# Performance work log

Hardware: AMD Instinct MI355X
Metric: run time of the kernel (lower is better)

The kernel has to match this reference:

```python
import jax, jax.numpy as jnp
import numpy as np

A, B, SDIM, ADIM, H, NH, DH = 15, 32768, 128, 32, 128, 4, 32
NEG = -1e9

def _lrelu(x):
    return jax.nn.leaky_relu(x, 0.01)

def setup_inputs() -> dict:
    key = jax.random.key(0)
    ks = jax.random.split(key, 14)
    w = lambda k, shp, s=0.05: jax.random.normal(k, shp, dtype=jnp.float32) * s
    return {
        'states': jax.random.normal(ks[0], (A, B, SDIM), dtype=jnp.float32),
        'actions': jax.random.normal(ks[1], (A, B, ADIM), dtype=jnp.float32),
        'Wenc': w(ks[2], (A, SDIM + ADIM, H)),
        'benc': w(ks[3], (A, H)),
        'Wsenc': w(ks[4], (A, SDIM, H)),
        'bsenc': w(ks[5], (A, H)),
        'Wk': w(ks[6], (NH, H, DH)),
        'Wsel': w(ks[7], (NH, H, DH)),
        'Wv': w(ks[8], (NH, H, DH)),
        'bv': w(ks[9], (NH, DH)),
        'Wc1': w(ks[10], (A, 2 * H, H)),
        'bc1': w(ks[11], (A, H)),
        'Wc2': w(ks[12], (A, H, ADIM)),
        'bc2': w(ks[13], (A, ADIM)),
    }

def reference(states, actions, Wenc, benc, Wsenc, bsenc, Wk, Wsel, Wv, bv, Wc1, bc1, Wc2, bc2):
    # per-agent (obs, act) encoders: [A,B,idim] x [A,idim,H] -> [A,B,H]
    sa = jnp.concatenate([states, actions], axis=-1)
    sa_enc = _lrelu(jnp.einsum('abi,aih->abh', sa, Wenc) + benc[:, None, :])
    s_enc = _lrelu(jnp.einsum('abs,ash->abh', states, Wsenc) + bsenc[:, None, :])
    # per-head key/value/selector projections (shared across agents)
    keys = jnp.einsum('jbe,ned->jbnd', sa_enc, Wk)                      # [A,B,NH,DH]
    vals = _lrelu(jnp.einsum('jbe,ned->jbnd', sa_enc, Wv) + bv[None, None])
    sel = jnp.einsum('ibe,ned->ibnd', s_enc, Wsel)                      # [A,B,NH,DH]
    # exclude-self attention over other agents
    logits = jnp.einsum('ibnd,jbnd->ibnj', sel, keys) / np.sqrt(DH).astype(np.float32)
    self_mask = jnp.eye(A, dtype=bool)[:, None, None, :]                # [A,1,1,A]
    probs = jax.nn.softmax(jnp.where(self_mask, NEG, logits), axis=-1)  # [A,B,NH,A]
    attn = jnp.einsum('ibnj,jbnd->ibnd', probs, vals)                   # [A,B,NH,DH]
    # per-agent critic head: cat(s_enc, all-head attention values) -> Q over actions
    critic_in = jnp.concatenate([s_enc, attn.reshape(A, B, NH * DH)], axis=-1)  # [A,B,2H]
    h = _lrelu(jnp.einsum('abi,aih->abh', critic_in, Wc1) + bc1[:, None, :])
    all_q = jnp.einsum('abh,aho->abo', h, Wc2) + bc2[:, None, :]        # [A,B,ADIM]
    return all_q
```

## Files before the change

kernel.cpp:

```cpp
#include <hip/hip_runtime.h>

typedef unsigned short u16;
typedef __attribute__((ext_vector_type(8))) short short8;
typedef __attribute__((ext_vector_type(4))) float f32x4;

#define NB 32768

__device__ __forceinline__ u16 f2bf(float x){
  unsigned int u = __float_as_uint(x);
  u += 0x7fffu + ((u >> 16) & 1u);
  return (u16)(u >> 16);
}
__device__ __forceinline__ float bf2f(short h){
  return __uint_as_float(((unsigned int)(u16)h) << 16);
}
__device__ __forceinline__ short8 pack8(float4 a, float4 b){
  short8 p;
  p[0]=(short)f2bf(a.x); p[1]=(short)f2bf(a.y); p[2]=(short)f2bf(a.z); p[3]=(short)f2bf(a.w);
  p[4]=(short)f2bf(b.x); p[5]=(short)f2bf(b.y); p[6]=(short)f2bf(b.z); p[7]=(short)f2bf(b.w);
  return p;
}

__global__ __launch_bounds__(256) void k0_conv(
    const float* __restrict__ Wenc, const float* __restrict__ Wsenc,
    const float* __restrict__ Wk, const float* __restrict__ Wsel, const float* __restrict__ Wv,
    const float* __restrict__ Wc1, const float* __restrict__ Wc2,
    u16* __restrict__ WencB, u16* __restrict__ WsencB,
    u16* __restrict__ WkB, u16* __restrict__ WvB, u16* __restrict__ WselB,
    u16* __restrict__ Wc1B, u16* __restrict__ Wc2B)
{
  int idx = blockIdx.x * 256 + threadIdx.x;
  if (idx < 307200){
    int a = idx / 20480, r = idx % 20480, n = r / 160, k = r % 160;
    WencB[idx] = f2bf(Wenc[a*20480 + k*128 + n]);
  } else if (idx < 552960){
    int i = idx - 307200; int a = i / 16384, r = i % 16384, n = r / 128, k = r % 128;
    WsencB[i] = f2bf(Wsenc[a*16384 + k*128 + n]);
  } else if (idx < 569344){
    int i = idx - 552960; int c = i / 128, k = i % 128;
    WkB[i] = f2bf(Wk[(c>>5)*4096 + k*32 + (c&31)]);
  } else if (idx < 585728){
    int i = idx - 569344; int c = i / 128, k = i % 128;
    WvB[i] = f2bf(Wv[(c>>5)*4096 + k*32 + (c&31)]);
  } else if (idx < 602112){
    int i = idx - 585728; int c = i / 128, k = i % 128;
    WselB[i] = f2bf(Wsel[(c>>5)*4096 + k*32 + (c&31)]);
  } else if (idx < 1093632){
    int i = idx - 602112; int a = i / 32768, r = i % 32768, n = r / 256, k = r % 256;
    Wc1B[i] = f2bf(Wc1[a*32768 + k*128 + n]);
  } else if (idx < 1155072){
    int i = idx - 1093632; int a = i / 4096, r = i % 4096, n = r / 128, k = r % 128;
    Wc2B[i] = f2bf(Wc2[a*4096 + k*32 + n]);
  }
}

__device__ __forceinline__ short8 ldA(const char* lds, int off, int row, int slot){
  return *(const short8*)(lds + off + row*256 + ((slot ^ (row & 7)) << 4));
}
__device__ __forceinline__ void stSwz(char* lds, int off, int row, int col, u16 v){
  *(u16*)(lds + off + row*256 + ((((col>>3) ^ (row&7))) << 4) + ((col&7) << 1)) = v;
}
#define MFMA(a8,b8,c) __builtin_amdgcn_mfma_f32_16x16x32_bf16(a8, b8, c, 0, 0, 0)

__device__ __forceinline__ void k1_gemm128(
    char* B, const short8* A0, const short8* A1, const u16* __restrict__ W,
    const float* __restrict__ bias, bool act, int l15, int l4)
{
  #pragma unroll
  for (int c = 0; c < 8; ++c){
    int col = c*16 + l15;
    const u16* Wn = W + (size_t)col*128;
    f32x4 a0 = (f32x4)0.f, a1 = (f32x4)0.f;
    #pragma unroll
    for (int ks = 0; ks < 4; ++ks){
      short8 b8 = *(const short8*)(Wn + ks*32 + l4*8);
      a0 = MFMA(A0[ks], b8, a0);
      a1 = MFMA(A1[ks], b8, a1);
    }
    float bb = bias ? bias[col] : 0.0f;
    #pragma unroll
    for (int q = 0; q < 4; ++q){
      float v0 = a0[q] + bb, v1 = a1[q] + bb;
      if (act){ v0 = v0 > 0.f ? v0 : 0.01f*v0; v1 = v1 > 0.f ? v1 : 0.01f*v1; }
      stSwz(B, 0, l4*4 + q,      col, f2bf(v0));
      stSwz(B, 0, 16 + l4*4 + q, col, f2bf(v1));
    }
  }
}
__device__ __forceinline__ void k1_copyout(const char* B, u16* __restrict__ dst,
                                           int a, int m0, int lane)
{
  #pragma unroll
  for (int it = 0; it < 8; ++it){
    int e = lane + it*64, row = e >> 4, cb = e & 15;
    *(short8*)(dst + ((size_t)a*NB + m0 + row)*128 + cb*8) =
        *(const short8*)(B + row*256 + ((cb ^ (row&7)) << 4));
  }
}

__global__ __launch_bounds__(256, 2) void k1_enc(
    const float* __restrict__ states, const float* __restrict__ actions,
    const float* __restrict__ benc, const float* __restrict__ bsenc, const float* __restrict__ bvp,
    const u16* __restrict__ WencB, const u16* __restrict__ WsencB,
    const u16* __restrict__ WkB, const u16* __restrict__ WvB, const u16* __restrict__ WselB,
    u16* __restrict__ se_g, u16* __restrict__ keys_g, u16* __restrict__ vals_g, u16* __restrict__ sel_g)
{
  extern __shared__ __align__(16) char lds[];
  const int a = blockIdx.y;
  const int w = threadIdx.x >> 6, lane = threadIdx.x & 63;
  const int l15 = lane & 15, l4 = lane >> 4;
  const int m0 = blockIdx.x*128 + w*32;
  char* B = lds + w*8192;

  short8 s0[4], s1[4], aa0, aa1;
  #pragma unroll
  for (int ks = 0; ks < 4; ++ks){
    const float* p0 = states + ((size_t)a*NB + m0 + l15)*128 + ks*32 + l4*8;
    s0[ks] = pack8(*(const float4*)p0, *(const float4*)(p0 + 4));
    const float* p1 = p0 + 16*128;
    s1[ks] = pack8(*(const float4*)p1, *(const float4*)(p1 + 4));
  }
  {
    const float* q0 = actions + ((size_t)a*NB + m0 + l15)*32 + l4*8;
    aa0 = pack8(*(const float4*)q0, *(const float4*)(q0 + 4));
    const float* q1 = q0 + 16*32;
    aa1 = pack8(*(const float4*)q1, *(const float4*)(q1 + 4));
  }

  k1_gemm128(B, s0, s1, WsencB + (size_t)a*16384, bsenc + a*128, true, l15, l4);
  k1_copyout(B, se_g, a, m0, lane);
  short8 seA0[4], seA1[4];
  #pragma unroll
  for (int ks = 0; ks < 4; ++ks){
    seA0[ks] = ldA(B, 0, l15,      ks*4 + l4);
    seA1[ks] = ldA(B, 0, 16 + l15, ks*4 + l4);
  }

  {
    const u16* We = WencB + (size_t)a*20480;
    const float* bi = benc + a*128;
    #pragma unroll
    for (int c = 0; c < 8; ++c){
      int col = c*16 + l15;
      const u16* Wn = We + (size_t)col*160;
      f32x4 a0 = (f32x4)0.f, a1 = (f32x4)0.f;
      #pragma unroll
      for (int ks = 0; ks < 4; ++ks){
        short8 b8 = *(const short8*)(Wn + ks*32 + l4*8);
        a0 = MFMA(s0[ks], b8, a0);
        a1 = MFMA(s1[ks], b8, a1);
      }
      short8 bt = *(const short8*)(Wn + 128 + l4*8);
      a0 = MFMA(aa0, bt, a0);
      a1 = MFMA(aa1, bt, a1);
      float bb = bi[col];
      #pragma unroll
      for (int q = 0; q < 4; ++q){
        float v0 = a0[q] + bb, v1 = a1[q] + bb;
        v0 = v0 > 0.f ? v0 : 0.01f*v0; v1 = v1 > 0.f ? v1 : 0.01f*v1;
        stSwz(B, 0, l4*4 + q,      col, f2bf(v0));
        stSwz(B, 0, 16 + l4*4 + q, col, f2bf(v1));
      }
    }
  }
  short8 saA0[4], saA1[4];
  #pragma unroll
  for (int ks = 0; ks < 4; ++ks){
    saA0[ks] = ldA(B, 0, l15,      ks*4 + l4);
    saA1[ks] = ldA(B, 0, 16 + l15, ks*4 + l4);
  }

  k1_gemm128(B, saA0, saA1, WkB, (const float*)nullptr, false, l15, l4);
  k1_copyout(B, keys_g, a, m0, lane);
  k1_gemm128(B, saA0, saA1, WvB, bvp, true, l15, l4);
  k1_copyout(B, vals_g, a, m0, lane);
  k1_gemm128(B, seA0, seA1, WselB, (const float*)nullptr, false, l15, l4);
  k1_copyout(B, sel_g, a, m0, lane);
}

#define KO 0
#define VO 61440
#define K2A_LDS 122880

__global__ __launch_bounds__(1024) void k2a_attn(
    const u16* __restrict__ keys_g, const u16* __restrict__ vals_g,
    const u16* __restrict__ sel_g, u16* __restrict__ attn_g)
{
  extern __shared__ __align__(16) char lds[];
  const int b0 = blockIdx.x * 16;
  const int t = threadIdx.x;
  const int lane = t & 63, w = t >> 6;
  const int b = lane >> 2, h = lane & 3;
  const bool act = w < 15;

  float sf[32];
  size_t base = 0;
  if (act){
    base = ((size_t)w*NB + b0 + b)*128 + h*32;
    #pragma unroll
    for (int x = 0; x < 4; ++x){
      short8 s8 = *(const short8*)(sel_g + base + x*8);
      #pragma unroll
      for (int y = 0; y < 8; ++y) sf[x*8+y] = bf2f(s8[y]);
    }
  }
  for (int e = t; e < 3840; e += 1024){
    int row = e >> 4, cb = e & 15;
    size_t src = ((size_t)(row >> 4)*NB + b0 + (row & 15))*128 + cb*8;
    int dst = row*256 + ((cb ^ (row&7)) << 4);
    *(short8*)(lds + KO + dst) = *(const short8*)(keys_g + src);
    *(short8*)(lds + VO + dst) = *(const short8*)(vals_g + src);
  }
  __syncthreads();

  if (act){
    float lg[15];
    #pragma unroll
    for (int j = 0; j < 15; ++j){
      int row = j*16 + b;
      float d = 0.f;
      #pragma unroll
      for (int x = 0; x < 4; ++x){
        short8 k8 = *(const short8*)(lds + KO + row*256 + (((h*4 + x) ^ (row&7)) << 4));
        #pragma unroll
        for (int y = 0; y < 8; ++y) d += bf2f(k8[y]) * sf[x*8+y];
      }
      lg[j] = d * 0.17677669529663687f;
    }
    float mx = -1e30f;
    #pragma unroll
    for (int j = 0; j < 15; ++j) if (j != w) mx = fmaxf(mx, lg[j]);
    float sum = 0.f;
    #pragma unroll
    for (int j = 0; j < 15; ++j){
      float p = (j == w) ? 0.f : __expf(lg[j] - mx);
      lg[j] = p; sum += p;
    }
    float inv = 1.f / sum;
    float oa[32];
    #pragma unroll
    for (int x = 0; x < 32; ++x) oa[x] = 0.f;
    #pragma unroll
    for (int j = 0; j < 15; ++j){
      if (j == w) continue;
      float p = lg[j];
      int row = j*16 + b;
      #pragma unroll
      for (int x = 0; x < 4; ++x){
        short8 v8 = *(const short8*)(lds + VO + row*256 + (((h*4 + x) ^ (row&7)) << 4));
        #pragma unroll
        for (int y = 0; y < 8; ++y) oa[x*8+y] += p * bf2f(v8[y]);
      }
    }
    #pragma unroll
    for (int x = 0; x < 4; ++x){
      short8 o;
      #pragma unroll
      for (int y = 0; y < 8; ++y) o[y] = (short)f2bf(oa[x*8+y] * inv);
      *(short8*)(attn_g + base + x*8) = o;
    }
  }
}

__global__ __launch_bounds__(256, 2) void k2b_critic(
    const u16* __restrict__ se_g, const u16* __restrict__ attn_g,
    const u16* __restrict__ Wc1B, const u16* __restrict__ Wc2B,
    const float* __restrict__ bc1, const float* __restrict__ bc2,
    float* __restrict__ outp)
{
  extern __shared__ __align__(16) char lds[];
  const int a = blockIdx.y;
  const int w = threadIdx.x >> 6, lane = threadIdx.x & 63;
  const int l15 = lane & 15, l4 = lane >> 4;
  const int m0 = blockIdx.x*128 + w*32;
  char* B = lds + w*8192;

  short8 se0[4], se1[4], at0[4], at1[4];
  #pragma unroll
  for (int ks = 0; ks < 4; ++ks){
    size_t o0 = ((size_t)a*NB + m0 + l15)*128 + ks*32 + l4*8;
    size_t o1 = o0 + 16*128;
    se0[ks] = *(const short8*)(se_g + o0);
    se1[ks] = *(const short8*)(se_g + o1);
    at0[ks] = *(const short8*)(attn_g + o0);
    at1[ks] = *(const short8*)(attn_g + o1);
  }
  {
    const u16* Wc = Wc1B + (size_t)a*32768;
    const float* bi = bc1 + a*128;
    #pragma unroll
    for (int c = 0; c < 8; ++c){
      int col = c*16 + l15;
      const u16* Wn = Wc + (size_t)col*256;
      f32x4 a0 = (f32x4)0.f, a1 = (f32x4)0.f;
      #pragma unroll
      for (int ks = 0; ks < 4; ++ks){
        short8 b8 = *(const short8*)(Wn + ks*32 + l4*8);
        a0 = MFMA(se0[ks], b8, a0);
        a1 = MFMA(se1[ks], b8, a1);
      }
      #pragma unroll
      for (int ks = 0; ks < 4; ++ks){
        short8 b8 = *(const short8*)(Wn + 128 + ks*32 + l4*8);
        a0 = MFMA(at0[ks], b8, a0);
        a1 = MFMA(at1[ks], b8, a1);
      }
      float bb = bi[col];
      #pragma unroll
      for (int q = 0; q < 4; ++q){
        float v0 = a0[q] + bb, v1 = a1[q] + bb;
        v0 = v0 > 0.f ? v0 : 0.01f*v0; v1 = v1 > 0.f ? v1 : 0.01f*v1;
        stSwz(B, 0, l4*4 + q,      col, f2bf(v0));
        stSwz(B, 0, 16 + l4*4 + q, col, f2bf(v1));
      }
    }
  }
  short8 h0[4], h1[4];
  #pragma unroll
  for (int ks = 0; ks < 4; ++ks){
    h0[ks] = ldA(B, 0, l15,      ks*4 + l4);
    h1[ks] = ldA(B, 0, 16 + l15, ks*4 + l4);
  }
  #pragma unroll
  for (int fn = 0; fn < 2; ++fn){
    int col = fn*16 + l15;
    const u16* Wn = Wc2B + (size_t)a*4096 + (size_t)col*128;
    f32x4 a0 = (f32x4)0.f, a1 = (f32x4)0.f;
    #pragma unroll
    for (int ks = 0; ks < 4; ++ks){
      short8 b8 = *(const short8*)(Wn + ks*32 + l4*8);
      a0 = MFMA(h0[ks], b8, a0);
      a1 = MFMA(h1[ks], b8, a1);
    }
    float bb = bc2[a*32 + col];
    #pragma unroll
    for (int q = 0; q < 4; ++q){
      outp[((size_t)a*NB + m0 + l4*4 + q)*32 + col]      = a0[q] + bb;
      outp[((size_t)a*NB + m0 + 16 + l4*4 + q)*32 + col] = a1[q] + bb;
    }
  }
}

extern "C" void kernel_launch(void* const* d_in, const int* in_sizes, int n_in,
                              void* d_out, int out_size, void* d_ws, size_t ws_size,
                              hipStream_t stream)
{
  const float* states  = (const float*)d_in[0];
  const float* actions = (const float*)d_in[1];
  const float* Wenc    = (const float*)d_in[2];
  const float* benc    = (const float*)d_in[3];
  const float* Wsenc   = (const float*)d_in[4];
  const float* bsenc   = (const float*)d_in[5];
  const float* Wk      = (const float*)d_in[6];
  const float* Wsel    = (const float*)d_in[7];
  const float* Wv      = (const float*)d_in[8];
  const float* bv      = (const float*)d_in[9];
  const float* Wc1     = (const float*)d_in[10];
  const float* bc1     = (const float*)d_in[11];
  const float* Wc2     = (const float*)d_in[12];
  const float* bc2     = (const float*)d_in[13];

  char* ws = (char*)d_ws;
  u16* WencB  = (u16*)(ws + 0);
  u16* WsencB = (u16*)(ws + 614400);
  u16* WkB    = (u16*)(ws + 1105920);
  u16* WvB    = (u16*)(ws + 1138688);
  u16* WselB  = (u16*)(ws + 1171456);
  u16* Wc1B   = (u16*)(ws + 1204224);
  u16* Wc2B   = (u16*)(ws + 2187264);
  u16* se_g   = (u16*)(ws + 2310144);
  u16* keys_g = (u16*)(ws + 128139264);
  u16* vals_g = (u16*)(ws + 253968384);
  u16* sel_g  = (u16*)(ws + 379797504);
  if (ws_size < 505626624ULL) return;

  hipFuncSetAttribute((const void*)k1_enc,     hipFuncAttributeMaxDynamicSharedMemorySize, 32768);
  hipFuncSetAttribute((const void*)k2a_attn,   hipFuncAttributeMaxDynamicSharedMemorySize, K2A_LDS);
  hipFuncSetAttribute((const void*)k2b_critic, hipFuncAttributeMaxDynamicSharedMemorySize, 32768);

  k0_conv<<<4512, 256, 0, stream>>>(Wenc, Wsenc, Wk, Wsel, Wv, Wc1, Wc2,
                                    WencB, WsencB, WkB, WvB, WselB, Wc1B, Wc2B);
  k1_enc<<<dim3(256, 15), 256, 32768, stream>>>(states, actions, benc, bsenc, bv,
                                                WencB, WsencB, WkB, WvB, WselB,
                                                se_g, keys_g, vals_g, sel_g);
  k2a_attn<<<2048, 1024, K2A_LDS, stream>>>(keys_g, vals_g, sel_g, keys_g);
  k2b_critic<<<dim3(256, 15), 256, 32768, stream>>>(se_g, keys_g, Wc1B, Wc2B,
                                                    bc1, bc2, (float*)d_out);
}
```

Baseline: 657.9 us.

## Stage encoder and projection weights in LDS shared across waves in k1_enc

In k1_enc each block now loads each weight matrix cooperatively into a swizzled LDS buffer, with a separate tail region for the action columns of Wenc, and all four waves read B operands from LDS instead of each wave fetching them from global/L2. The GEMMs are reordered so the selector projection runs right after the state encoder, which frees the register arrays that held s_enc. The aim is to cut redundant weight traffic and register pressure. In exchange the kernel adds several block-wide barriers and raises LDS to 72KB per block, which may limit how many blocks fit per CU.

```diff
diff --git a/kernel.cpp b/kernel.cpp
--- a/kernel.cpp
+++ b/kernel.cpp
@@ -14,6 +14,7 @@
 __device__ __forceinline__ float bf2f(short h){
   return __uint_as_float(((unsigned int)(u16)h) << 16);
 }
+__device__ __forceinline__ float lrelu(float v){ return v > 0.f ? v : 0.01f*v; }
 __device__ __forceinline__ short8 pack8(float4 a, float4 b){
   short8 p;
   p[0]=(short)f2bf(a.x); p[1]=(short)f2bf(a.y); p[2]=(short)f2bf(a.z); p[3]=(short)f2bf(a.w);
@@ -62,18 +63,35 @@
 }
 #define MFMA(a8,b8,c) __builtin_amdgcn_mfma_f32_16x16x32_bf16(a8, b8, c, 0, 0, 0)
 
-__device__ __forceinline__ void k1_gemm128(
-    char* B, const short8* A0, const short8* A1, const u16* __restrict__ W,
+#define WBUF 0
+#define WTAIL 32768
+#define BOUNCE 40960
+#define K1_LDS 73728
+
+__device__ __forceinline__ void stageW(char* lds, const u16* __restrict__ W, int ldk, int t){
+  #pragma unroll
+  for (int i = 0; i < 8; ++i){
+    int e = t + i*256;
+    int col = e >> 4, slot = e & 15;
+    *(short8*)(lds + WBUF + col*256 + ((slot ^ (col&7)) << 4)) =
+        *(const short8*)(W + (size_t)col*ldk + slot*8);
+  }
+}
+__device__ __forceinline__ short8 ldB(const char* lds, int col, int slot){
+  return *(const short8*)(lds + WBUF + col*256 + ((slot ^ (col&7)) << 4));
+}
+
+__device__ __forceinline__ void gemm2L(
+    char* B, const char* lds, const short8* A0, const short8* A1,
     const float* __restrict__ bias, bool act, int l15, int l4)
 {
   #pragma unroll
   for (int c = 0; c < 8; ++c){
     int col = c*16 + l15;
-    const u16* Wn = W + (size_t)col*128;
     f32x4 a0 = (f32x4)0.f, a1 = (f32x4)0.f;
     #pragma unroll
     for (int ks = 0; ks < 4; ++ks){
-      short8 b8 = *(const short8*)(Wn + ks*32 + l4*8);
+      short8 b8 = ldB(lds, col, ks*4 + l4);
       a0 = MFMA(A0[ks], b8, a0);
       a1 = MFMA(A1[ks], b8, a1);
     }
@@ -81,7 +99,7 @@
     #pragma unroll
     for (int q = 0; q < 4; ++q){
       float v0 = a0[q] + bb, v1 = a1[q] + bb;
-      if (act){ v0 = v0 > 0.f ? v0 : 0.01f*v0; v1 = v1 > 0.f ? v1 : 0.01f*v1; }
+      if (act){ v0 = lrelu(v0); v1 = lrelu(v1); }
       stSwz(B, 0, l4*4 + q,      col, f2bf(v0));
       stSwz(B, 0, 16 + l4*4 + q, col, f2bf(v1));
     }
@@ -107,12 +125,13 @@
 {
   extern __shared__ __align__(16) char lds[];
   const int a = blockIdx.y;
-  const int w = threadIdx.x >> 6, lane = threadIdx.x & 63;
+  const int t = threadIdx.x;
+  const int w = t >> 6, lane = t & 63;
   const int l15 = lane & 15, l4 = lane >> 4;
   const int m0 = blockIdx.x*128 + w*32;
-  char* B = lds + w*8192;
-
-  short8 s0[4], s1[4], aa0, aa1;
+  char* B = lds + BOUNCE + w*8192;
+
+  short8 s0[4], s1[4];
   #pragma unroll
   for (int ks = 0; ks < 4; ++ks){
     const float* p0 = states + ((size_t)a*NB + m0 + l15)*128 + ks*32 + l4*8;
@@ -120,62 +139,81 @@
     const float* p1 = p0 + 16*128;
     s1[ks] = pack8(*(const float4*)p1, *(const float4*)(p1 + 4));
   }
+
+  short8 T0[4], T1[4];
+
+  stageW(lds, WsencB + (size_t)a*16384, 128, t);
+  __syncthreads();
+  gemm2L(B, lds, s0, s1, bsenc + a*128, true, l15, l4);
+  k1_copyout(B, se_g, a, m0, lane);
+  #pragma unroll
+  for (int ks = 0; ks < 4; ++ks){
+    T0[ks] = ldA(B, 0, l15,      ks*4 + l4);
+    T1[ks] = ldA(B, 0, 16 + l15, ks*4 + l4);
+  }
+  __syncthreads();
+
+  stageW(lds, WselB, 128, t);
+  __syncthreads();
+  gemm2L(B, lds, T0, T1, (const float*)nullptr, false, l15, l4);
+  k1_copyout(B, sel_g, a, m0, lane);
+  __syncthreads();
+
+  stageW(lds, WencB + (size_t)a*20480, 160, t);
+  #pragma unroll
+  for (int i = 0; i < 2; ++i){
+    int e = t + i*256;
+    int col = e >> 2, sl = e & 3;
+    *(short8*)(lds + WTAIL + col*64 + ((sl ^ (col&3)) << 4)) =
+        *(const short8*)(WencB + (size_t)a*20480 + (size_t)col*160 + 128 + sl*8);
+  }
+  __syncthreads();
   {
+    short8 aa0, aa1;
     const float* q0 = actions + ((size_t)a*NB + m0 + l15)*32 + l4*8;
     aa0 = pack8(*(const float4*)q0, *(const float4*)(q0 + 4));
     const float* q1 = q0 + 16*32;
     aa1 = pack8(*(const float4*)q1, *(const float4*)(q1 + 4));
-  }
-
-  k1_gemm128(B, s0, s1, WsencB + (size_t)a*16384, bsenc + a*128, true, l15, l4);
-  k1_copyout(B, se_g, a, m0, lane);
-  short8 seA0[4], seA1[4];
-  #pragma unroll
-  for (int ks = 0; ks < 4; ++ks){
-    seA0[ks] = ldA(B, 0, l15,      ks*4 + l4);
-    seA1[ks] = ldA(B, 0, 16 + l15, ks*4 + l4);
-  }
-
-  {
-    const u16* We = WencB + (size_t)a*20480;
     const float* bi = benc + a*128;
     #pragma unroll
     for (int c = 0; c < 8; ++c){
       int col = c*16 + l15;
-      const u16* Wn = We + (size_t)col*160;
       f32x4 a0 = (f32x4)0.f, a1 = (f32x4)0.f;
       #pragma unroll
       for (int ks = 0; ks < 4; ++ks){
-        short8 b8 = *(const short8*)(Wn + ks*32 + l4*8);
+        short8 b8 = ldB(lds, col, ks*4 + l4);
         a0 = MFMA(s0[ks], b8, a0);
         a1 = MFMA(s1[ks], b8, a1);
       }
-      short8 bt = *(const short8*)(Wn + 128 + l4*8);
+      short8 bt = *(const short8*)(lds + WTAIL + col*64 + ((l4 ^ (col&3)) << 4));
       a0 = MFMA(aa0, bt, a0);
       a1 = MFMA(aa1, bt, a1);
       float bb = bi[col];
       #pragma unroll
       for (int q = 0; q < 4; ++q){
         float v0 = a0[q] + bb, v1 = a1[q] + bb;
-        v0 = v0 > 0.f ? v0 : 0.01f*v0; v1 = v1 > 0.f ? v1 : 0.01f*v1;
-        stSwz(B, 0, l4*4 + q,      col, f2bf(v0));
-        stSwz(B, 0, 16 + l4*4 + q, col, f2bf(v1));
-      }
-    }
-  }
-  short8 saA0[4], saA1[4];
+        stSwz(B, 0, l4*4 + q,      col, f2bf(lrelu(v0)));
+        stSwz(B, 0, 16 + l4*4 + q, col, f2bf(lrelu(v1)));
+      }
+    }
+  }
   #pragma unroll
   for (int ks = 0; ks < 4; ++ks){
-    saA0[ks] = ldA(B, 0, l15,      ks*4 + l4);
-    saA1[ks] = ldA(B, 0, 16 + l15, ks*4 + l4);
-  }
-
-  k1_gemm128(B, saA0, saA1, WkB, (const float*)nullptr, false, l15, l4);
+    T0[ks] = ldA(B, 0, l15,      ks*4 + l4);
+    T1[ks] = ldA(B, 0, 16 + l15, ks*4 + l4);
+  }
+  __syncthreads();
+
+  stageW(lds, WkB, 128, t);
+  __syncthreads();
+  gemm2L(B, lds, T0, T1, (const float*)nullptr, false, l15, l4);
   k1_copyout(B, keys_g, a, m0, lane);
-  k1_gemm128(B, saA0, saA1, WvB, bvp, true, l15, l4);
+  __syncthreads();
+
+  stageW(lds, WvB, 128, t);
+  __syncthreads();
+  gemm2L(B, lds, T0, T1, bvp, true, l15, l4);
   k1_copyout(B, vals_g, a, m0, lane);
-  k1_gemm128(B, seA0, seA1, WselB, (const float*)nullptr, false, l15, l4);
-  k1_copyout(B, sel_g, a, m0, lane);
 }
 
 #define KO 0
@@ -309,7 +347,7 @@
       #pragma unroll
       for (int q = 0; q < 4; ++q){
         float v0 = a0[q] + bb, v1 = a1[q] + bb;
-        v0 = v0 > 0.f ? v0 : 0.01f*v0; v1 = v1 > 0.f ? v1 : 0.01f*v1;
+        v0 = lrelu(v0); v1 = lrelu(v1);
         stSwz(B, 0, l4*4 + q,      col, f2bf(v0));
         stSwz(B, 0, 16 + l4*4 + q, col, f2bf(v1));
       }
@@ -374,15 +412,15 @@
   u16* sel_g  = (u16*)(ws + 379797504);
   if (ws_size < 505626624ULL) return;
 
-  hipFuncSetAttribute((const void*)k1_enc,     hipFuncAttributeMaxDynamicSharedMemorySize, 32768);
+  hipFuncSetAttribute((const void*)k1_enc,     hipFuncAttributeMaxDynamicSharedMemorySize, K1_LDS);
   hipFuncSetAttribute((const void*)k2a_attn,   hipFuncAttributeMaxDynamicSharedMemorySize, K2A_LDS);
   hipFuncSetAttribute((const void*)k2b_critic, hipFuncAttributeMaxDynamicSharedMemorySize, 32768);
 
   k0_conv<<<4512, 256, 0, stream>>>(Wenc, Wsenc, Wk, Wsel, Wv, Wc1, Wc2,
                                     WencB, WsencB, WkB, WvB, WselB, Wc1B, Wc2B);
-  k1_enc<<<dim3(256, 15), 256, 32768, stream>>>(states, actions, benc, bsenc, bv,
-                                                WencB, WsencB, WkB, WvB, WselB,
-                                                se_g, keys_g, vals_g, sel_g);
+  k1_enc<<<dim3(256, 15), 256, K1_LDS, stream>>>(states, actions, benc, bsenc, bv,
+                                                 WencB, WsencB, WkB, WvB, WselB,
+                                                 se_g, keys_g, vals_g, sel_g);
   k2a_attn<<<2048, 1024, K2A_LDS, stream>>>(keys_g, vals_g, sel_g, keys_g);
   k2b_critic<<<dim3(256, 15), 256, 32768, stream>>>(se_g, keys_g, Wc1B, Wc2B,
                                                     bc1, bc2, (float*)d_out);
```

Measured after the change: 659.6 us. About the same (+0.3%).

## Chunk batch into four passes to keep intermediates cache-resident; restructure encoder GEMMs

Applied to the files above, without the earlier changes.

The batch is split into four chunks of 8192 rows, and the encoder, attention and critic kernels run per chunk on a smaller scratch buffer. The goal is for the bf16 intermediates (se, keys, vals, sel) to stay in the large last-level cache between kernels instead of round-tripping through HBM. The encoder GEMMs now accumulate four column tiles at once in a non-unrolled loop, and states are reloaded to cut live registers, so occupancy can rise to 4 blocks per CU. The cost is three times more kernel launches, smaller grids per launch, and an extra read of states.

```diff
diff --git a/kernel.cpp b/kernel.cpp
--- a/kernel.cpp
+++ b/kernel.cpp
@@ -5,6 +5,8 @@
 typedef __attribute__((ext_vector_type(4))) float f32x4;
 
 #define NB 32768
+#define CHB 8192
+#define NCH 4
 
 __device__ __forceinline__ u16 f2bf(float x){
   unsigned int u = __float_as_uint(x);
@@ -14,6 +16,7 @@
 __device__ __forceinline__ float bf2f(short h){
   return __uint_as_float(((unsigned int)(u16)h) << 16);
 }
+__device__ __forceinline__ float lrelu(float v){ return v > 0.f ? v : 0.01f*v; }
 __device__ __forceinline__ short8 pack8(float4 a, float4 b){
   short8 p;
   p[0]=(short)f2bf(a.x); p[1]=(short)f2bf(a.y); p[2]=(short)f2bf(a.z); p[3]=(short)f2bf(a.w);
@@ -62,120 +65,142 @@
 }
 #define MFMA(a8,b8,c) __builtin_amdgcn_mfma_f32_16x16x32_bf16(a8, b8, c, 0, 0, 0)
 
-__device__ __forceinline__ void k1_gemm128(
-    char* B, const short8* A0, const short8* A1, const u16* __restrict__ W,
+#define K1_LDS 32768
+
+__device__ __forceinline__ void gemm2c(
+    char* B, const short8* A0, const short8* A1, const u16* __restrict__ W, int ldk,
     const float* __restrict__ bias, bool act, int l15, int l4)
 {
-  #pragma unroll
-  for (int c = 0; c < 8; ++c){
-    int col = c*16 + l15;
-    const u16* Wn = W + (size_t)col*128;
-    f32x4 a0 = (f32x4)0.f, a1 = (f32x4)0.f;
-    #pragma unroll
-    for (int ks = 0; ks < 4; ++ks){
-      short8 b8 = *(const short8*)(Wn + ks*32 + l4*8);
-      a0 = MFMA(A0[ks], b8, a0);
-      a1 = MFMA(A1[ks], b8, a1);
-    }
-    float bb = bias ? bias[col] : 0.0f;
-    #pragma unroll
-    for (int q = 0; q < 4; ++q){
-      float v0 = a0[q] + bb, v1 = a1[q] + bb;
-      if (act){ v0 = v0 > 0.f ? v0 : 0.01f*v0; v1 = v1 > 0.f ? v1 : 0.01f*v1; }
-      stSwz(B, 0, l4*4 + q,      col, f2bf(v0));
-      stSwz(B, 0, 16 + l4*4 + q, col, f2bf(v1));
+  #pragma unroll 1
+  for (int cg = 0; cg < 2; ++cg){
+    f32x4 a0[4], a1[4];
+    #pragma unroll
+    for (int cc = 0; cc < 4; ++cc){ a0[cc] = (f32x4)0.f; a1[cc] = (f32x4)0.f; }
+    #pragma unroll
+    for (int ks = 0; ks < 4; ++ks)
+      #pragma unroll
+      for (int cc = 0; cc < 4; ++cc){
+        int col = cg*64 + cc*16 + l15;
+        short8 b8 = *(const short8*)(W + (size_t)col*ldk + ks*32 + l4*8);
+        a0[cc] = MFMA(A0[ks], b8, a0[cc]);
+        a1[cc] = MFMA(A1[ks], b8, a1[cc]);
+      }
+    #pragma unroll
+    for (int cc = 0; cc < 4; ++cc){
+      int col = cg*64 + cc*16 + l15;
+      float bb = bias ? bias[col] : 0.0f;
+      #pragma unroll
+      for (int q = 0; q < 4; ++q){
+        float v0 = a0[cc][q] + bb, v1 = a1[cc][q] + bb;
+        if (act){ v0 = lrelu(v0); v1 = lrelu(v1); }
+        stSwz(B, 0, l4*4 + q,      col, f2bf(v0));
+        stSwz(B, 0, 16 + l4*4 + q, col, f2bf(v1));
+      }
     }
   }
 }
 __device__ __forceinline__ void k1_copyout(const char* B, u16* __restrict__ dst,
-                                           int a, int m0, int lane)
+                                           int a, int m0c, int lane)
 {
   #pragma unroll
   for (int it = 0; it < 8; ++it){
     int e = lane + it*64, row = e >> 4, cb = e & 15;
-    *(short8*)(dst + ((size_t)a*NB + m0 + row)*128 + cb*8) =
+    *(short8*)(dst + ((size_t)a*CHB + m0c + row)*128 + cb*8) =
         *(const short8*)(B + row*256 + ((cb ^ (row&7)) << 4));
   }
 }
 
-__global__ __launch_bounds__(256, 2) void k1_enc(
-    const float* __restrict__ states, const float* __restrict__ actions,
+__global__ __launch_bounds__(256, 4) void k1_enc(
+    const float* __restrict__ states, const float* __restrict__ actions, int base,
     const float* __restrict__ benc, const float* __restrict__ bsenc, const float* __restrict__ bvp,
     const u16* __restrict__ WencB, const u16* __restrict__ WsencB,
     const u16* __restrict__ WkB, const u16* __restrict__ WvB, const u16* __restrict__ WselB,
-    u16* __restrict__ se_g, u16* __restrict__ keys_g, u16* __restrict__ vals_g, u16* __restrict__ sel_g)
+    u16* __restrict__ se_c, u16* __restrict__ keys_c, u16* __restrict__ vals_c, u16* __restrict__ sel_c)
 {
   extern __shared__ __align__(16) char lds[];
   const int a = blockIdx.y;
-  const int w = threadIdx.x >> 6, lane = threadIdx.x & 63;
+  const int t = threadIdx.x;
+  const int w = t >> 6, lane = t & 63;
   const int l15 = lane & 15, l4 = lane >> 4;
-  const int m0 = blockIdx.x*128 + w*32;
+  const int m0c = blockIdx.x*128 + w*32;
+  const int m0g = base + m0c;
   char* B = lds + w*8192;
 
-  short8 s0[4], s1[4], aa0, aa1;
+  short8 T0[4], T1[4];
+
+  {
+    short8 s0[4], s1[4];
+    #pragma unroll
+    for (int ks = 0; ks < 4; ++ks){
+      const float* p0 = states + ((size_t)a*NB + m0g + l15)*128 + ks*32 + l4*8;
+      s0[ks] = pack8(*(const float4*)p0, *(const float4*)(p0 + 4));
+      const float* p1 = p0 + 16*128;
+      s1[ks] = pack8(*(const float4*)p1, *(const float4*)(p1 + 4));
+    }
+    gemm2c(B, s0, s1, WsencB + (size_t)a*16384, 128, bsenc + a*128, true, l15, l4);
+  }
+  k1_copyout(B, se_c, a, m0c, lane);
   #pragma unroll
   for (int ks = 0; ks < 4; ++ks){
-    const float* p0 = states + ((size_t)a*NB + m0 + l15)*128 + ks*32 + l4*8;
-    s0[ks] = pack8(*(const float4*)p0, *(const float4*)(p0 + 4));
-    const float* p1 = p0 + 16*128;
-    s1[ks] = pack8(*(const float4*)p1, *(const float4*)(p1 + 4));
-  }
+    T0[ks] = ldA(B, 0, l15,      ks*4 + l4);
+    T1[ks] = ldA(B, 0, 16 + l15, ks*4 + l4);
+  }
+  gemm2c(B, T0, T1, WselB, 128, (const float*)nullptr, false, l15, l4);
+  k1_copyout(B, sel_c, a, m0c, lane);
+
   {
-    const float* q0 = actions + ((size_t)a*NB + m0 + l15)*32 + l4*8;
+    short8 s0[4], s1[4], aa0, aa1;
+    #pragma unroll
+    for (int ks = 0; ks < 4; ++ks){
+      const float* p0 = states + ((size_t)a*NB + m0g + l15)*128 + ks*32 + l4*8;
+      s0[ks] = pack8(*(const float4*)p0, *(const float4*)(p0 + 4));
+      const float* p1 = p0 + 16*128;
+      s1[ks] = pack8(*(const float4*)p1, *(const float4*)(p1 + 4));
+    }
+    const float* q0 = actions + ((size_t)a*NB + m0g + l15)*32 + l4*8;
     aa0 = pack8(*(const float4*)q0, *(const float4*)(q0 + 4));
     const float* q1 = q0 + 16*32;
     aa1 = pack8(*(const float4*)q1, *(const float4*)(q1 + 4));
-  }
-
-  k1_gemm128(B, s0, s1, WsencB + (size_t)a*16384, bsenc + a*128, true, l15, l4);
-  k1_copyout(B, se_g, a, m0, lane);
-  short8 seA0[4], seA1[4];
-  #pragma unroll
-  for (int ks = 0; ks < 4; ++ks){
-    seA0[ks] = ldA(B, 0, l15,      ks*4 + l4);
-    seA1[ks] = ldA(B, 0, 16 + l15, ks*4 + l4);
-  }
-
-  {
     const u16* We = WencB + (size_t)a*20480;
     const float* bi = benc + a*128;
-    #pragma unroll
-    for (int c = 0; c < 8; ++c){
-      int col = c*16 + l15;
-      const u16* Wn = We + (size_t)col*160;
-      f32x4 a0 = (f32x4)0.f, a1 = (f32x4)0.f;
-      #pragma unroll
-      for (int ks = 0; ks < 4; ++ks){
-        short8 b8 = *(const short8*)(Wn + ks*32 + l4*8);
-        a0 = MFMA(s0[ks], b8, a0);
-        a1 = MFMA(s1[ks], b8, a1);
-      }
-      short8 bt = *(const short8*)(Wn + 128 + l4*8);
-      a0 = MFMA(aa0, bt, a0);
-      a1 = MFMA(aa1, bt, a1);
-      float bb = bi[col];
-      #pragma unroll
-      for (int q = 0; q < 4; ++q){
-        float v0 = a0[q] + bb, v1 = a1[q] + bb;
-        v0 = v0 > 0.f ? v0 : 0.01f*v0; v1 = v1 > 0.f ? v1 : 0.01f*v1;
-        stSwz(B, 0, l4*4 + q,      col, f2bf(v0));
-        stSwz(B, 0, 16 + l4*4 + q, col, f2bf(v1));
-      }
-    }
-  }
-  short8 saA0[4], saA1[4];
+    #pragma unroll 1
+    for (int cg = 0; cg < 2; ++cg){
+      f32x4 a0[4], a1[4];
+      #pragma unroll
+      for (int cc = 0; cc < 4; ++cc){ a0[cc] = (f32x4)0.f; a1[cc] = (f32x4)0.f; }
+      #pragma unroll
+      for (int ks = 0; ks < 4; ++ks)
+        #pragma unroll
+        for (int cc = 0; cc < 4; ++cc){
+          int col = cg*64 + cc*16 + l15;
+          short8 b8 = *(const short8*)(We + (size_t)col*160 + ks*32 + l4*8);
+          a0[cc] = MFMA(s0[ks], b8, a0[cc]);
+          a1[cc] = MFMA(s1[ks], b8, a1[cc]);
+        }
+      #pragma unroll
+      for (int cc = 0; cc < 4; ++cc){
+        int col = cg*64 + cc*16 + l15;
+        short8 bt = *(const short8*)(We + (size_t)col*160 + 128 + l4*8);
+        a0[cc] = MFMA(aa0, bt, a0[cc]);
+        a1[cc] = MFMA(aa1, bt, a1[cc]);
+        float bb = bi[col];
+        #pragma unroll
+        for (int q = 0; q < 4; ++q){
+          stSwz(B, 0, l4*4 + q,      col, f2bf(lrelu(a0[cc][q] + bb)));
+          stSwz(B, 0, 16 + l4*4 + q, col, f2bf(lrelu(a1[cc][q] + bb)));
+        }
+      }
+    }
+  }
   #pragma unroll
   for (int ks = 0; ks < 4; ++ks){
-    saA0[ks] = ldA(B, 0, l15,      ks*4 + l4);
-    saA1[ks] = ldA(B, 0, 16 + l15, ks*4 + l4);
-  }
-
-  k1_gemm128(B, saA0, saA1, WkB, (const float*)nullptr, false, l15, l4);
-  k1_copyout(B, keys_g, a, m0, lane);
-  k1_gemm128(B, saA0, saA1, WvB, bvp, true, l15, l4);
-  k1_copyout(B, vals_g, a, m0, lane);
-  k1_gemm128(B, seA0, seA1, WselB, (const float*)nullptr, false, l15, l4);
-  k1_copyout(B, sel_g, a, m0, lane);
+    T0[ks] = ldA(B, 0, l15,      ks*4 + l4);
+    T1[ks] = ldA(B, 0, 16 + l15, ks*4 + l4);
+  }
+  gemm2c(B, T0, T1, WkB, 128, (const float*)nullptr, false, l15, l4);
+  k1_copyout(B, keys_c, a, m0c, lane);
+  gemm2c(B, T0, T1, WvB, 128, bvp, true, l15, l4);
+  k1_copyout(B, vals_c, a, m0c, lane);
 }
 
 #define KO 0
@@ -183,8 +208,8 @@
 #define K2A_LDS 122880
 
 __global__ __launch_bounds__(1024) void k2a_attn(
-    const u16* __restrict__ keys_g, const u16* __restrict__ vals_g,
-    const u16* __restrict__ sel_g, u16* __restrict__ attn_g)
+    const u16* __restrict__ keys_c, const u16* __restrict__ vals_c,
+    const u16* __restrict__ sel_c, u16* __restrict__ attn_c)
 {
   extern __shared__ __align__(16) char lds[];
   const int b0 = blockIdx.x * 16;
@@ -196,20 +221,20 @@
   float sf[32];
   size_t base = 0;
   if (act){
-    base = ((size_t)w*NB + b0 + b)*128 + h*32;
+    base = ((size_t)w*CHB + b0 + b)*128 + h*32;
     #pragma unroll
     for (int x = 0; x < 4; ++x){
-      short8 s8 = *(const short8*)(sel_g + base + x*8);
+      short8 s8 = *(const short8*)(sel_c + base + x*8);
       #pragma unroll
       for (int y = 0; y < 8; ++y) sf[x*8+y] = bf2f(s8[y]);
     }
   }
   for (int e = t; e < 3840; e += 1024){
     int row = e >> 4, cb = e & 15;
-    size_t src = ((size_t)(row >> 4)*NB + b0 + (row & 15))*128 + cb*8;
+    size_t src = ((size_t)(row >> 4)*CHB + b0 + (row & 15))*128 + cb*8;
     int dst = row*256 + ((cb ^ (row&7)) << 4);
-    *(short8*)(lds + KO + dst) = *(const short8*)(keys_g + src);
-    *(short8*)(lds + VO + dst) = *(const short8*)(vals_g + src);
+    *(short8*)(lds + KO + dst) = *(const short8*)(keys_c + src);
+    *(short8*)(lds + VO + dst) = *(const short8*)(vals_c + src);
   }
   __syncthreads();
 
@@ -257,33 +282,33 @@
       short8 o;
       #pragma unroll
       for (int y = 0; y < 8; ++y) o[y] = (short)f2bf(oa[x*8+y] * inv);
-      *(short8*)(attn_g + base + x*8) = o;
+      *(short8*)(attn_c + base + x*8) = o;
     }
   }
 }
 
 __global__ __launch_bounds__(256, 2) void k2b_critic(
-    const u16* __restrict__ se_g, const u16* __restrict__ attn_g,
+    const u16* __restrict__ se_c, const u16* __restrict__ attn_c,
     const u16* __restrict__ Wc1B, const u16* __restrict__ Wc2B,
     const float* __restrict__ bc1, const float* __restrict__ bc2,
-    float* __restrict__ outp)
+    int base, float* __restrict__ outp)
 {
   extern __shared__ __align__(16) char lds[];
   const int a = blockIdx.y;
   const int w = threadIdx.x >> 6, lane = threadIdx.x & 63;
   const int l15 = lane & 15, l4 = lane >> 4;
-  const int m0 = blockIdx.x*128 + w*32;
+  const int m0c = blockIdx.x*128 + w*32;
   char* B = lds + w*8192;
 
   short8 se0[4], se1[4], at0[4], at1[4];
   #pragma unroll
   for (int ks = 0; ks < 4; ++ks){
-    size_t o0 = ((size_t)a*NB + m0 + l15)*128 + ks*32 + l4*8;
+    size_t o0 = ((size_t)a*CHB + m0c + l15)*128 + ks*32 + l4*8;
     size_t o1 = o0 + 16*128;
-    se0[ks] = *(const short8*)(se_g + o0);
-    se1[ks] = *(const short8*)(se_g + o1);
-    at0[ks] = *(const short8*)(attn_g + o0);
-    at1[ks] = *(const short8*)(attn_g + o1);
+    se0[ks] = *(const short8*)(se_c + o0);
+    se1[ks] = *(const short8*)(se_c + o1);
+    at0[ks] = *(const short8*)(attn_c + o0);
+    at1[ks] = *(const short8*)(attn_c + o1);
   }
   {
     const u16* Wc = Wc1B + (size_t)a*32768;
@@ -308,10 +333,8 @@
       float bb = bi[col];
       #pragma unroll
       for (int q = 0; q < 4; ++q){
-        float v0 = a0[q] + bb, v1 = a1[q] + bb;
-        v0 = v0 > 0.f ? v0 : 0.01f*v0; v1 = v1 > 0.f ? v1 : 0.01f*v1;
-        stSwz(B, 0, l4*4 + q,      col, f2bf(v0));
-        stSwz(B, 0, 16 + l4*4 + q, col, f2bf(v1));
+        stSwz(B, 0, l4*4 + q,      col, f2bf(lrelu(a0[q] + bb)));
+        stSwz(B, 0, 16 + l4*4 + q, col, f2bf(lrelu(a1[q] + bb)));
       }
     }
   }
@@ -335,8 +358,8 @@
     float bb = bc2[a*32 + col];
     #pragma unroll
     for (int q = 0; q < 4; ++q){
-      outp[((size_t)a*NB + m0 + l4*4 + q)*32 + col]      = a0[q] + bb;
-      outp[((size_t)a*NB + m0 + 16 + l4*4 + q)*32 + col] = a1[q] + bb;
+      outp[((size_t)a*NB + base + m0c + l4*4 + q)*32 + col]      = a0[q] + bb;
+      outp[((size_t)a*NB + base + m0c + 16 + l4*4 + q)*32 + col] = a1[q] + bb;
     }
   }
 }
@@ -368,22 +391,26 @@
   u16* WselB  = (u16*)(ws + 1171456);
   u16* Wc1B   = (u16*)(ws + 1204224);
   u16* Wc2B   = (u16*)(ws + 2187264);
-  u16* se_g   = (u16*)(ws + 2310144);
-  u16* keys_g = (u16*)(ws + 128139264);
-  u16* vals_g = (u16*)(ws + 253968384);
-  u16* sel_g  = (u16*)(ws + 379797504);
-  if (ws_size < 505626624ULL) return;
-
-  hipFuncSetAttribute((const void*)k1_enc,     hipFuncAttributeMaxDynamicSharedMemorySize, 32768);
+  u16* se_c   = (u16*)(ws + 2310144);
+  u16* keys_c = (u16*)(ws + 33767424);
+  u16* vals_c = (u16*)(ws + 65224704);
+  u16* sel_c  = (u16*)(ws + 96681984);
+  if (ws_size < 128139264ULL) return;
+
+  hipFuncSetAttribute((const void*)k1_enc,     hipFuncAttributeMaxDynamicSharedMemorySize, K1_LDS);
   hipFuncSetAttribute((const void*)k2a_attn,   hipFuncAttributeMaxDynamicSharedMemorySize, K2A_LDS);
   hipFuncSetAttribute((const void*)k2b_critic, hipFuncAttributeMaxDynamicSharedMemorySize, 32768);
 
   k0_conv<<<4512, 256, 0, stream>>>(Wenc, Wsenc, Wk, Wsel, Wv, Wc1, Wc2,
                                     WencB, WsencB, WkB, WvB, WselB, Wc1B, Wc2B);
-  k1_enc<<<dim3(256, 15), 256, 32768, stream>>>(states, actions, benc, bsenc, bv,
-                                                WencB, WsencB, WkB, WvB, WselB,
-                                                se_g, keys_g, vals_g, sel_g);
-  k2a_attn<<<2048, 1024, K2A_LDS, stream>>>(keys_g, vals_g, sel_g, keys_g);
-  k2b_critic<<<dim3(256, 15), 256, 32768, stream>>>(se_g, keys_g, Wc1B, Wc2B,
-                                                    bc1, bc2, (float*)d_out);
-}
+  for (int ch = 0; ch < NCH; ++ch){
+    int base = ch * CHB;
+    k1_enc<<<dim3(CHB/128, 15), 256, K1_LDS, stream>>>(states, actions, base,
+                                                       benc, bsenc, bv,
+                                                       WencB, WsencB, WkB, WvB, WselB,
+                                                       se_c, keys_c, vals_c, sel_c);
+    k2a_attn<<<CHB/16, 1024, K2A_LDS, stream>>>(keys_c, vals_c, sel_c, keys_c);
+    k2b_critic<<<dim3(CHB/128, 15), 256, 32768, stream>>>(se_c, keys_c, Wc1B, Wc2B,
+                                                          bc1, bc2, base, (float*)d_out);
+  }
+}
```

Result: slower. 778.1 us (+18.3%).
